# Kernel tuning notes

Measured on AMD Instinct MI355X. Metric: run time of the kernel, lower is better.

## Reference

```python
import math
import jax, jax.numpy as jnp
import numpy as np

SR = 48000.0
HARMONIC_NUM = 8
SINE_AMP = 0.1
NOISE_STD = 0.003


def setup_inputs() -> dict:
    key = jax.random.key(0)
    k1, k2, k3 = jax.random.split(key, 3)
    B, T = 16, 400
    H = HARMONIC_NUM
    # F0 contour in Hz, uniform [0, 400)
    f0 = jax.random.uniform(k1, (B, T), dtype=jnp.float32) * 400.0
    # tiny merge linear: (harmonic_num+1) -> 1
    W = jax.random.normal(k2, (1, H + 1), dtype=jnp.float32) * (1.0 / math.sqrt(H + 1))
    b = jax.random.normal(k3, (1,), dtype=jnp.float32) * 0.01
    return {"f0": f0, "upp": 512, "W": W, "b": b}


def reference(f0, upp, W, b):
    # f0: (B, T) Hz -> nearest-neighbor upsample by integer factor upp: (B, Tu, 1)
    f0_up = jnp.repeat(f0, upp, axis=1)[..., None]
    rad = f0_up / SR  # normalized freq per sample, (B, Tu, 1)
    # multipliers 1..H+1: fundamental + harmonics 2..H+1 (torch uses rad*(k+1), k=1..H)
    m = jnp.arange(1, HARMONIC_NUM + 2, dtype=f0.dtype)  # (H+1,)
    phase = jnp.cumsum(rad * m, axis=1) * jnp.asarray(2.0 * math.pi, f0.dtype)
    sine_waves = jnp.sin(phase) * SINE_AMP  # (B, Tu, H+1)
    uv = (f0_up > 1.0).astype(f0.dtype)  # (B, Tu, 1)
    noise_amp = uv * NOISE_STD + (1.0 - uv) * (SINE_AMP / 3.0)
    noise = noise_amp * jax.random.normal(jax.random.key(42), sine_waves.shape, sine_waves.dtype)
    src = sine_waves * uv + noise  # (B, Tu, H+1)
    out = jnp.tanh(src @ W.T + b)  # (B, Tu, 1)
    return jnp.transpose(out, (0, 2, 1))  # (B, 1, Tu)
```

## Files before the change

### kernel.cpp

```cpp
#include <hip/hip_runtime.h>
#include <math.h>
#include <stdint.h>

#define NB 16
#define NT 400
#define UPP 512
#define TUP (NT * UPP)
#define NH 9
#define NSAMP (NB * TUP)
#define SPT 4
#define THREADS (UPP / SPT)

__device__ __forceinline__ uint32_t rotl32(uint32_t x, uint32_t d) {
  return (x << d) | (x >> (32u - d));
}

__device__ __forceinline__ void tf2x32_multi(uint32_t* x0, uint32_t* x1) {
  const uint32_t ks1 = 42u;
  const uint32_t ks2 = 0x1BD11BDAu ^ 0u ^ 42u;
#define TFRN(r)                                                      \
  _Pragma("unroll") for (int i = 0; i < SPT; ++i) {                  \
    x0[i] += x1[i]; x1[i] = rotl32(x1[i], r); x1[i] ^= x0[i];        \
  }
#define INJN(a, b)                                                   \
  _Pragma("unroll") for (int i = 0; i < SPT; ++i) {                  \
    x0[i] += (a); x1[i] += (b);                                      \
  }
  INJN(0u, ks1)
  TFRN(13) TFRN(15) TFRN(26) TFRN(6)
  INJN(ks1, ks2 + 1u)
  TFRN(17) TFRN(29) TFRN(16) TFRN(24)
  INJN(ks2, 0u + 2u)
  TFRN(13) TFRN(15) TFRN(26) TFRN(6)
  INJN(0u, ks1 + 3u)
  TFRN(17) TFRN(29) TFRN(16) TFRN(24)
  INJN(ks1, ks2 + 4u)
  TFRN(13) TFRN(15) TFRN(26) TFRN(6)
  INJN(ks2, 0u + 5u)
#undef TFRN
#undef INJN
}

#if defined(__has_builtin)
#if __has_builtin(__builtin_amdgcn_sinf)
#define HW_SIN_REV(x) __builtin_amdgcn_sinf(x)
#endif
#if __has_builtin(__builtin_amdgcn_cosf)
#define HW_COS_REV(x) __builtin_amdgcn_cosf(x)
#endif
#if __has_builtin(__builtin_amdgcn_fractf)
#define FRACT_F32(x) __builtin_amdgcn_fractf(x)
#endif
#if __has_builtin(__builtin_amdgcn_logf)
#define HW_LOG2(x) __builtin_amdgcn_logf(x)
#endif
#if __has_builtin(__builtin_amdgcn_sqrtf)
#define HW_SQRT(x) __builtin_amdgcn_sqrtf(x)
#endif
#endif
#ifndef HW_SIN_REV
#define HW_SIN_REV(x) __sinf(6.283185307179586f * (x))
#endif
#ifndef HW_COS_REV
#define HW_COS_REV(x) __cosf(6.283185307179586f * (x))
#endif
#ifndef FRACT_F32
#define FRACT_F32(x) ((x) - floorf(x))
#endif
#ifndef HW_LOG2
#define HW_LOG2(x) __log2f(x)
#endif
#ifndef HW_SQRT
#define HW_SQRT(x) __fsqrt_rn(x)
#endif

__device__ __forceinline__ float pu_main(uint32_t bits, float& L, float& u) {
  float f = __uint_as_float((bits >> 9) | 0x3f800000u) - 1.0f;
  const float lo = -0.99999994f;
  float uu = fmaf(f, 2.0f, lo);
  uu = fmaxf(uu, lo);
  u = uu;
  float x2 = (1.0f - uu) * (1.0f + uu);
  L = HW_LOG2(x2);
  float w = fmaf(-0.69314718f, L, -2.5f);
  float p = 2.81022636e-08f;
  p = fmaf(p, w, 3.43273939e-07f);
  p = fmaf(p, w, -3.5233877e-06f);
  p = fmaf(p, w, -4.39150654e-06f);
  p = fmaf(p, w, 0.00021858087f);
  p = fmaf(p, w, -0.00125372503f);
  p = fmaf(p, w, -0.00417768164f);
  p = fmaf(p, w, 0.246640727f);
  p = fmaf(p, w, 1.50140941f);
  return p;
}

__device__ __forceinline__ float pu_tail(float L) {
  float t = HW_SQRT(-0.69314718f * L) - 3.0f;
  float q = -0.000200214257f;
  q = fmaf(q, t, 0.000100950558f);
  q = fmaf(q, t, 0.00134934322f);
  q = fmaf(q, t, -0.00367342844f);
  q = fmaf(q, t, 0.00573950773f);
  q = fmaf(q, t, -0.0076224613f);
  q = fmaf(q, t, 0.00943887047f);
  q = fmaf(q, t, 1.00167406f);
  q = fmaf(q, t, 2.83297682f);
  return q;
}

__global__ __launch_bounds__(THREADS) void snsf_main(
    const float* __restrict__ f0, const float* __restrict__ W,
    const float* __restrict__ bptr, float* __restrict__ out) {
  constexpr int NWAVE = THREADS / 64;
  __shared__ double spart[NWAVE];

  int fb = blockIdx.x;
  int bb = fb / NT;
  int j  = fb - bb * NT;
  int r  = threadIdx.x;

  const float* row = f0 + bb * NT;
  double v = 0.0;
#pragma unroll
  for (int k = 0; k < (NT + THREADS - 1) / THREADS; ++k) {
    int idx = r + k * THREADS;
    if (idx < j) v += (double)row[idx];
  }
#pragma unroll
  for (int off = 32; off >= 1; off >>= 1) v += __shfl_xor(v, off);
  if ((r & 63) == 0) spart[r >> 6] = v;
  __syncthreads();
  double sum = 0.0;
#pragma unroll
  for (int wv = 0; wv < NWAVE; ++wv) sum += spart[wv];
  double tphase = sum * (512.0 / 48000.0);
  float B0v = (float)(tphase - floor(tphase));

  float f0v = row[j];
  float rad = f0v * (1.0f / 48000.0f);
  bool uv = f0v > 1.0f;
  float ampP = uv ? 0.0042426409f : 0.047140453f;
  float samp = uv ? 0.1f : 0.0f;

  int t0 = SPT * r;
  int s0 = bb * TUP + (j << 9) + t0;

  float z[SPT], zp[SPT], c2[SPT], pre[SPT];
#pragma unroll
  for (int i = 0; i < SPT; ++i) {
    float th = fmaf((float)(t0 + i + 1), rad, B0v);
    float fr = FRACT_F32(th);
    z[i] = HW_SIN_REV(fr);
    float c = HW_COS_REV(fr);
    c2[i] = c + c;
    zp[i] = 0.0f;
    pre[i] = bptr[0];
  }

  uint32_t base9 = 9u * (uint32_t)s0;
#pragma unroll
  for (int h = 0; h < NH; ++h) {
    uint32_t x0[SPT], x1[SPT];
#pragma unroll
    for (int i = 0; i < SPT; ++i) {
      x0[i] = 0u;
      x1[i] = base9 + (uint32_t)(9 * i + h);
    }
    tf2x32_multi(x0, x1);
    float L[SPT], u[SPT], p[SPT];
    bool anytail = false;
#pragma unroll
    for (int i = 0; i < SPT; ++i) {
      p[i] = pu_main(x0[i] ^ x1[i], L[i], u[i]);
      anytail = anytail || (L[i] <= -7.2134752f);
    }
    if (__builtin_expect(__any(anytail), 0)) {
#pragma unroll
      for (int i = 0; i < SPT; ++i)
        if (L[i] <= -7.2134752f) p[i] = pu_tail(L[i]);
    }
#pragma unroll
    for (int i = 0; i < SPT; ++i) {
      float pu = p[i] * u[i];
      float srcv = fmaf(samp, z[i], ampP * pu);
      pre[i] = fmaf(W[h], srcv, pre[i]);
      float zn = fmaf(c2[i], z[i], -zp[i]);
      zp[i] = z[i];
      z[i] = zn;
    }
  }

  float o[SPT];
#pragma unroll
  for (int i = 0; i < SPT; ++i) {
    float x2v = pre[i] * pre[i];
    o[i] = pre[i] * fmaf(x2v, fmaf(x2v, 0.13333334f, -0.33333334f), 1.0f);
  }
  *reinterpret_cast<float4*>(out + s0) = make_float4(o[0], o[1], o[2], o[3]);
}

extern "C" void kernel_launch(void* const* d_in, const int* in_sizes, int n_in,
                              void* d_out, int out_size, void* d_ws, size_t ws_size,
                              hipStream_t stream) {
  const float* f0 = (const float*)d_in[0];
  const float* W = (const float*)d_in[2];
  const float* b = (const float*)d_in[3];
  float* out = (float*)d_out;

  snsf_main<<<dim3(NB * NT), dim3(THREADS), 0, stream>>>(f0, W, b, out);
}
```

Baseline: 125.9 us.

## Process two frames per 512-thread block with two samples per thread

Each block now covers two consecutive frames using 512 threads, and each thread computes two samples instead of four. The per-frame prefix sum of f0 is shared by both halves, and the second half adds the first frame's f0. This doubles the number of threads and cuts per-thread register use to raise parallelism and latency hiding. In exchange, each thread keeps less instruction-level parallelism in the Threefry interleave and uses narrower float2 stores.

```diff
diff --git a/kernel.cpp b/kernel.cpp
--- a/kernel.cpp
+++ b/kernel.cpp
@@ -8,14 +8,13 @@
 #define TUP (NT * UPP)
 #define NH 9
 #define NSAMP (NB * TUP)
-#define SPT 4
-#define THREADS (UPP / SPT)
+#define SPT 2
 
 __device__ __forceinline__ uint32_t rotl32(uint32_t x, uint32_t d) {
   return (x << d) | (x >> (32u - d));
 }
 
-__device__ __forceinline__ void tf2x32_multi(uint32_t* x0, uint32_t* x1) {
+__device__ __forceinline__ void tf2x32_dual(uint32_t* x0, uint32_t* x1) {
   const uint32_t ks1 = 42u;
   const uint32_t ks2 = 0x1BD11BDAu ^ 0u ^ 42u;
 #define TFRN(r)                                                      \
@@ -109,31 +108,29 @@
   return q;
 }
 
-__global__ __launch_bounds__(THREADS) void snsf_main(
+__global__ __launch_bounds__(512) void snsf_main(
     const float* __restrict__ f0, const float* __restrict__ W,
     const float* __restrict__ bptr, float* __restrict__ out) {
-  constexpr int NWAVE = THREADS / 64;
-  __shared__ double spart[NWAVE];
-
-  int fb = blockIdx.x;
-  int bb = fb / NT;
-  int j  = fb - bb * NT;
+  __shared__ double spart[8];
+
+  int pb = blockIdx.x;
+  int bb = pb / (NT / 2);
+  int jp = pb - bb * (NT / 2);
+  int j0 = jp * 2;
   int r  = threadIdx.x;
+  int half = r >> 8;
+  int rr = r & 255;
+  int j  = j0 + half;
 
   const float* row = f0 + bb * NT;
-  double v = 0.0;
-#pragma unroll
-  for (int k = 0; k < (NT + THREADS - 1) / THREADS; ++k) {
-    int idx = r + k * THREADS;
-    if (idx < j) v += (double)row[idx];
-  }
+  double v = (r < j0) ? (double)row[r] : 0.0;
 #pragma unroll
   for (int off = 32; off >= 1; off >>= 1) v += __shfl_xor(v, off);
   if ((r & 63) == 0) spart[r >> 6] = v;
   __syncthreads();
-  double sum = 0.0;
-#pragma unroll
-  for (int wv = 0; wv < NWAVE; ++wv) sum += spart[wv];
+  double sum = spart[0] + spart[1] + spart[2] + spart[3] +
+               spart[4] + spart[5] + spart[6] + spart[7];
+  if (half) sum += (double)row[j0];
   double tphase = sum * (512.0 / 48000.0);
   float B0v = (float)(tphase - floor(tphase));
 
@@ -143,7 +140,7 @@
   float ampP = uv ? 0.0042426409f : 0.047140453f;
   float samp = uv ? 0.1f : 0.0f;
 
-  int t0 = SPT * r;
+  int t0 = SPT * rr;
   int s0 = bb * TUP + (j << 9) + t0;
 
   float z[SPT], zp[SPT], c2[SPT], pre[SPT];
@@ -167,7 +164,7 @@
       x0[i] = 0u;
       x1[i] = base9 + (uint32_t)(9 * i + h);
     }
-    tf2x32_multi(x0, x1);
+    tf2x32_dual(x0, x1);
     float L[SPT], u[SPT], p[SPT];
     bool anytail = false;
 #pragma unroll
@@ -197,7 +194,7 @@
     float x2v = pre[i] * pre[i];
     o[i] = pre[i] * fmaf(x2v, fmaf(x2v, 0.13333334f, -0.33333334f), 1.0f);
   }
-  *reinterpret_cast<float4*>(out + s0) = make_float4(o[0], o[1], o[2], o[3]);
+  *reinterpret_cast<float2*>(out + s0) = make_float2(o[0], o[1]);
 }
 
 extern "C" void kernel_launch(void* const* d_in, const int* in_sizes, int n_in,
@@ -208,5 +205,5 @@
   const float* b = (const float*)d_in[3];
   float* out = (float*)d_out;
 
-  snsf_main<<<dim3(NB * NT), dim3(THREADS), 0, stream>>>(f0, W, b, out);
-}
+  snsf_main<<<dim3(NB * NT / 2), dim3(512), 0, stream>>>(f0, W, b, out);
+}
```

Measured after the change: 125.5 us. Within noise of the previous version (-0.3%).
